# Performance work log

Measured on AMD Instinct MI355X. Metric: run time of the kernel, lower is better.

The kernel has to match this reference:

```python
import jax, jax.numpy as jnp
import numpy as np

D = 256            # number of graph nodes (example.size(3))
K1 = D // 2        # topkpool1 k
K2 = D // 4        # topkpool2 k
B = 8


def _lrelu(x):
    return jnp.where(x > 0, x, 0.33 * x)


def _e2e(h, wa, ba, wb, bb):
    # h: [B,C,d,d]; wa,wb: [P,C,d] (squeezed (1,d)/(d,1) conv kernels)
    # cnn1: contract over columns j -> [B,P,d]; cnn2: contract over rows i -> [B,P,d]
    a = jnp.einsum('bcij,pcj->bpi', h, wa) + ba[None, :, None]
    b = jnp.einsum('bcij,pci->bpj', h, wb) + bb[None, :, None]
    # cat([a]*d, 3) + cat([b]*d, 2)  ==  broadcast-add
    return a[:, :, :, None] + b[:, :, None, :]


def _gcn(h, g, W, b):
    # h: [B,N,F_in], g: [B,N,N]; faithful to norm_g: g[i,j] / deg[j] (column-normalized
    # because torch broadcasts the [N] degree vector over the LAST dim)
    gb = (g > 0).astype(h.dtype)
    deg = gb.sum(axis=2)                      # [B,N] row sums
    gn = gb / deg[:, None, :]                 # divide column j by deg[j]
    return jnp.einsum('bij,bjf->bif', gn, h) @ W.T + b


def _pool(h, g, s, k):
    # h: [B,N,F], g: [B,N,N], s: [B,N,1] -> top-k nodes by score (descending)
    vals, idx = jax.lax.top_k(s[:, :, 0], k)              # [B,k]
    hn = jnp.take_along_axis(h, idx[:, :, None], axis=1)  # [B,k,F]
    gn = jnp.take_along_axis(g, idx[:, :, None], axis=1)
    gn = jnp.take_along_axis(gn, idx[:, None, :], axis=2) # [B,k,k]
    return hn, gn, vals[:, :, None]


def _readout(h):
    # h: [B,N,F] (node axis = 1); torch ReadOut on [B,F,N,1] max/mean over dim=2
    return jnp.concatenate([h.max(axis=1), h.mean(axis=1)], axis=1)  # [B,2F]


def _forward(x, w1a, b1a, w1b, b1b, w2a, b2a, w2b, b2b, e2n_w, e2n_b,
             a11_w, a11_b, a12_w, a12_b, g1_w, g1_b,
             a21_w, a21_b, a22_w, a22_b,
             d1_w, d1_b, d2_w, d2_b, d3_w, d3_b):
    h = _lrelu(_e2e(x, w1a, b1a, w1b, b1b))         # [B,128,d,d]
    h = _lrelu(_e2e(h, w2a, b2a, w2b, b2b))         # [B,256,d,d]
    # E2N conv (1,d): [B,8,d,1] -> node features [B,d,8]
    nodes = _lrelu(jnp.einsum('bcij,pcj->bpi', h, e2n_w) + e2n_b[None, :, None])
    nodes = jnp.transpose(nodes, (0, 2, 1))          # [B,d,8]
    g0 = x[:, 0]                                     # [B,d,d]

    w = _lrelu(_gcn(nodes, g0, a11_w, a11_b))        # [B,d,1]
    w = jax.nn.sigmoid(_gcn(w, g0, a12_w, a12_b))
    h1, g1, s1 = _pool(nodes, g0, w, K1)             # [B,K1,8], [B,K1,K1], [B,K1,1]
    out = h1 * s1 + h1
    sum1 = _readout(out)                             # [B,16]

    h2 = _gcn(out, g1, g1_w, g1_b)                   # [B,K1,8] (no activation, as in torch)
    w = _lrelu(_gcn(h2, g1, a21_w, a21_b))
    w = jax.nn.sigmoid(_gcn(w, g1, a22_w, a22_b))
    h3, g2, s2 = _pool(h2, g1, w, K2)                # [B,K2,8]
    out2 = h3 * s2 + h3
    sum2 = _readout(out2)                            # [B,16]

    z = sum1 + sum2                                  # [B,16]
    z = _lrelu(z @ d1_w.T + d1_b)                    # dropout = identity (eval mode)
    z = _lrelu(z @ d2_w.T + d2_b)
    return z @ d3_w.T + d3_b                         # [B,1]


def setup_inputs() -> dict:
    key = jax.random.key(0)
    ks = jax.random.split(key, 16)
    f32 = jnp.float32

    def rn(k, shape, scale):
        return jax.random.normal(k, shape, dtype=f32) * scale

    return {
        'x': jax.random.normal(ks[0], (B, 1, D, D), dtype=f32),
        'w1a': rn(ks[1], (128, 1, D), 0.08),  'b1a': jnp.zeros((128,), f32),
        'w1b': rn(ks[2], (128, 1, D), 0.08),  'b1b': jnp.zeros((128,), f32),
        'w2a': rn(ks[3], (256, 128, D), 0.008), 'b2a': jnp.zeros((256,), f32),
        'w2b': rn(ks[4], (256, 128, D), 0.008), 'b2b': jnp.zeros((256,), f32),
        'e2n_w': rn(ks[5], (8, 256, D), 0.005), 'e2n_b': jnp.zeros((8,), f32),
        'a11_w': rn(ks[6], (1, 8), 0.3),  'a11_b': jnp.zeros((1,), f32),
        'a12_w': rn(ks[7], (1, 1), 0.3),  'a12_b': jnp.zeros((1,), f32),
        'g1_w': rn(ks[8], (8, 8), 0.3),   'g1_b': jnp.zeros((8,), f32),
        'a21_w': rn(ks[9], (1, 8), 0.3),  'a21_b': jnp.zeros((1,), f32),
        'a22_w': rn(ks[10], (1, 1), 0.3), 'a22_b': jnp.zeros((1,), f32),
        'd1_w': rn(ks[11], (128, 16), 0.2), 'd1_b': jnp.zeros((128,), f32),
        'd2_w': rn(ks[12], (64, 128), 0.08), 'd2_b': jnp.zeros((64,), f32),
        'd3_w': rn(ks[13], (1, 64), 0.1),  'd3_b': jnp.zeros((1,), f32),
    }


def reference(x, w1a, b1a, w1b, b1b, w2a, b2a, w2b, b2b, e2n_w, e2n_b,
              a11_w, a11_b, a12_w, a12_b, g1_w, g1_b,
              a21_w, a21_b, a22_w, a22_b,
              d1_w, d1_b, d2_w, d2_b, d3_w, d3_b):
    return _forward(x, w1a, b1a, w1b, b1b, w2a, b2a, w2b, b2b, e2n_w, e2n_b,
                    a11_w, a11_b, a12_w, a12_b, g1_w, g1_b,
                    a21_w, a21_b, a22_w, a22_b,
                    d1_w, d1_b, d2_w, d2_b, d3_w, d3_b)
```

## Files before the change

kernel.cpp:

```cpp
#include <hip/hip_runtime.h>

typedef short s16x8 __attribute__((ext_vector_type(8)));
typedef float f32x4 __attribute__((ext_vector_type(4)));
typedef float f32x2 __attribute__((ext_vector_type(2)));

#define TID threadIdx.x

__device__ __forceinline__ float lrelu_f(float x) { return fmaxf(x, 0.33f * x); }

__device__ __forceinline__ unsigned lrelu_pack(float pv, f32x2 q) {
    f32x2 s = q + pv;
    f32x2 m = s * 0.33f;
    f32x2 r = __builtin_elementwise_max(s, m);
    unsigned u;
    asm("v_cvt_pk_bf16_f32 %0, %1, %2" : "=v"(u) : "v"(r.x), "v"(r.y));
    return u;
}
__device__ __forceinline__ unsigned pk_bf16(float a, float b) {
    unsigned u;
    asm("v_cvt_pk_bf16_f32 %0, %1, %2" : "=v"(u) : "v"(a), "v"(b));
    return u;
}

union FragU { s16x8 v; uint4 q; unsigned w[4]; };

__global__ __launch_bounds__(256) void k_convert(
    const float* __restrict__ sa, unsigned short* __restrict__ da, int na4,
    const float* __restrict__ sb, unsigned short* __restrict__ db, int nb4,
    const float* __restrict__ sc, unsigned short* __restrict__ dc, int nc4)
{
    const float* s; unsigned short* d; int n4;
    if (blockIdx.y == 0)      { s = sa; d = da; n4 = na4; }
    else if (blockIdx.y == 1) { s = sb; d = db; n4 = nb4; }
    else                      { s = sc; d = dc; n4 = nc4; }
    const int stride = gridDim.x * 256;
    for (int i = blockIdx.x * 256 + TID; i < n4; i += stride) {
        float4 v = ((const float4*)s)[i];
        ((uint2*)d)[i] = make_uint2(pk_bf16(v.x, v.y), pk_bf16(v.z, v.w));
    }
}

__global__ __launch_bounds__(128) void k_l1(
    const float* __restrict__ x,
    const float* __restrict__ w1a, const float* __restrict__ b1a,
    const float* __restrict__ w1b, const float* __restrict__ b1b,
    float* __restrict__ A1, float* __restrict__ B1)
{
    const int r = blockIdx.x, b = blockIdx.y, v = blockIdx.z;
    const int tid = TID;
    __shared__ float xr[256];
    const float* xb = x + b * 65536;
    if (v == 0) {
        xr[tid]       = xb[r * 256 + tid];
        xr[tid + 128] = xb[r * 256 + tid + 128];
    } else {
        xr[tid]       = xb[tid * 256 + r];
        xr[tid + 128] = xb[(tid + 128) * 256 + r];
    }
    __syncthreads();
    const float* w    = v ? w1b : w1a;
    const float* bias = v ? b1b : b1a;
    float* OUT = v ? B1 : A1;
    float acc = bias[tid];
    const float* wr = w + tid * 256;
    #pragma unroll 4
    for (int q = 0; q < 256; q += 8) {
        float4 a = *(const float4*)(wr + q);
        float4 c = *(const float4*)(wr + q + 4);
        acc += xr[q + 0] * a.x + xr[q + 1] * a.y + xr[q + 2] * a.z + xr[q + 3] * a.w;
        acc += xr[q + 4] * c.x + xr[q + 5] * c.y + xr[q + 6] * c.z + xr[q + 7] * c.w;
    }
    OUT[b * 32768 + tid * 256 + r] = acc;
}

__global__ __launch_bounds__(512, 4) void k_e2e(
    const float* __restrict__ A1, const float* __restrict__ B1,
    const unsigned short* __restrict__ w2aM, const unsigned short* __restrict__ w2bM,
    float* __restrict__ part)
{
    const int bid = blockIdx.x;
    const int xcd = bid & 7, tt = bid >> 3;
    const int hi = tt >> 5, inner = tt & 31;
    const int slice = xcd + 8 * hi;
    const int s = slice >> 1, which = slice & 1;
    const int rt = inner >> 3, b = inner & 7;
    const int bw = b * 2 + which;

    const float* P = (which ? B1 : A1) + b * 32768;
    const float* Q = (which ? A1 : B1) + b * 32768;
    const unsigned short* W = which ? w2bM : w2aM;
    const int c0 = s * 16, r0 = rt * 64;

    __shared__ float Qs[16][256];
    __shared__ float Ps[16][64];
    __shared__ uint4 Hs[2048];

    const int tid = TID;
    const int wave = tid >> 6, lane = tid & 63, quad = lane >> 4, l16 = lane & 15;
    const int pbase = wave * 32;

    {
        const float4* Qg = (const float4*)(Q + c0 * 256);
        float4* Qd = (float4*)&Qs[0][0];
        Qd[tid]       = Qg[tid];
        Qd[tid + 512] = Qg[tid + 512];
        int row = tid >> 5, c2 = (tid & 31) * 2;
        *(float2*)&Ps[row][c2] = *(const float2*)&P[(c0 + row) * 256 + r0 + c2];
    }
    __syncthreads();

    {
        const int qb = wave * 32 + quad * 8;
        f32x2 qp0 = *(const f32x2*)&Qs[0][qb + 0];
        f32x2 qp1 = *(const f32x2*)&Qs[0][qb + 2];
        f32x2 qp2 = *(const f32x2*)&Qs[0][qb + 4];
        f32x2 qp3 = *(const f32x2*)&Qs[0][qb + 6];
        #pragma unroll
        for (int rf = 0; rf < 4; ++rf) {
            float pv = Ps[0][rf * 16 + l16];
            uint4 u;
            u.x = lrelu_pack(pv, qp0);
            u.y = lrelu_pack(pv, qp1);
            u.z = lrelu_pack(pv, qp2);
            u.w = lrelu_pack(pv, qp3);
            Hs[(wave * 4 + rf) * 64 + lane] = u;
        }
    }

    f32x4 acc[2][4] = {};
    const unsigned short* Wrow[2];
    #pragma unroll
    for (int pf = 0; pf < 2; ++pf)
        Wrow[pf] = W + (size_t)(pbase + pf * 16 + l16) * 32768 + c0 * 256 + quad * 8;

    FragU af[2][2];
    #pragma unroll
    for (int pf = 0; pf < 2; ++pf) af[0][pf].q = *(const uint4*)(Wrow[pf]);

    __syncthreads();

    for (int c = 0; c < 16; ++c) {
        FragU hbf[2][4];
        #pragma unroll
        for (int nf = 0; nf < 4; ++nf)
            hbf[0][nf].q = Hs[nf * 64 + lane];

        #pragma unroll
        for (int q0 = 0; q0 < 8; ++q0) {
            const int cur = q0 & 1, nxt = cur ^ 1;
            const int cn = c + ((q0 + 1) >> 3), qn = (q0 + 1) & 7;
            if (cn < 16) {
                #pragma unroll
                for (int pf = 0; pf < 2; ++pf)
                    af[nxt][pf].q = *(const uint4*)(Wrow[pf] + cn * 256 + qn * 32);
            }
            if (q0 < 7) {
                #pragma unroll
                for (int nf = 0; nf < 4; ++nf)
                    hbf[nxt][nf].q = Hs[((q0 + 1) * 4 + nf) * 64 + lane];
            }
            #pragma unroll
            for (int nf = 0; nf < 4; ++nf)
                #pragma unroll
                for (int pf = 0; pf < 2; ++pf)
                    acc[pf][nf] = __builtin_amdgcn_mfma_f32_16x16x32_bf16(af[cur][pf].v, hbf[cur][nf].v, acc[pf][nf], 0, 0, 0);
        }
        __syncthreads();
        if (c + 1 < 16) {
            const int qb = wave * 32 + quad * 8;
            f32x2 qp0 = *(const f32x2*)&Qs[c + 1][qb + 0];
            f32x2 qp1 = *(const f32x2*)&Qs[c + 1][qb + 2];
            f32x2 qp2 = *(const f32x2*)&Qs[c + 1][qb + 4];
            f32x2 qp3 = *(const f32x2*)&Qs[c + 1][qb + 6];
            #pragma unroll
            for (int rf = 0; rf < 4; ++rf) {
                float pv = Ps[c + 1][rf * 16 + l16];
                uint4 u;
                u.x = lrelu_pack(pv, qp0);
                u.y = lrelu_pack(pv, qp1);
                u.z = lrelu_pack(pv, qp2);
                u.w = lrelu_pack(pv, qp3);
                Hs[(wave * 4 + rf) * 64 + lane] = u;
            }
            __syncthreads();
        }
    }

    float* pb = part + (size_t)(s * 16 + bw) * 65536;
    #pragma unroll
    for (int pf = 0; pf < 2; ++pf)
        #pragma unroll
        for (int nf = 0; nf < 4; ++nf)
            #pragma unroll
            for (int t = 0; t < 4; ++t) {
                int p = pbase + pf * 16 + quad * 4 + t;
                int r = r0 + nf * 16 + l16;
                pb[p * 256 + r] = acc[pf][nf][t];
            }
}

__global__ __launch_bounds__(256) void k_red(
    const float* __restrict__ part,
    const float* __restrict__ b2a, const float* __restrict__ b2b,
    float* __restrict__ A2, float* __restrict__ B2)
{
    const int bw = blockIdx.y; const int b = bw >> 1, which = bw & 1;
    const int idx = blockIdx.x * 256 + TID;
    const float4* pp = (const float4*)part;
    float4 acc = make_float4(0.f, 0.f, 0.f, 0.f);
    #pragma unroll
    for (int s = 0; s < 8; ++s) {
        float4 v = pp[(size_t)(s * 16 + bw) * 16384 + idx];
        acc.x += v.x; acc.y += v.y; acc.z += v.z; acc.w += v.w;
    }
    const int p = idx >> 6;
    const float bias = (which ? b2b : b2a)[p];
    acc.x += bias; acc.y += bias; acc.z += bias; acc.w += bias;
    float* OUT = (which ? B2 : A2) + b * 65536;
    ((float4*)OUT)[idx] = acc;
}

__global__ __launch_bounds__(256) void k_e2n(
    const float* __restrict__ A2, const float* __restrict__ B2,
    const unsigned short* __restrict__ e2nw,
    float* __restrict__ nodes_raw)
{
    const int it = blockIdx.x, b = blockIdx.y, sn = blockIdx.z;
    const int tid = TID, wave = tid >> 6, lane = tid & 63, quad = lane >> 4, l16 = lane & 15;
    const int i0 = it * 16;
    const int c0 = sn * 32 + wave * 8;
    const float* Ab = A2 + b * 65536;
    const float* Bb = B2 + b * 65536;
    const float* Brow0 = Bb + c0 * 256 + quad * 8;
    const unsigned short* Wrow0 = e2nw + (size_t)l16 * 65536 + c0 * 256 + quad * 8;

    f32x4 acc = {};
    FragU af[2];
    f32x2 qp[2][4];
    float pv, pvn;

    if (l16 < 8) af[0].q = *(const uint4*)(Wrow0);
    else         af[0].q = make_uint4(0u, 0u, 0u, 0u);
    #pragma unroll
    for (int k = 0; k < 4; ++k) qp[0][k] = *(const f32x2*)(Brow0 + 2 * k);
    pv = Ab[c0 * 256 + i0 + l16];

    for (int cc = 0; cc < 8; ++cc) {
        #pragma unroll
        for (int q0 = 0; q0 < 8; ++q0) {
            const int cur = q0 & 1, nxt = cur ^ 1;
            const int cn = (q0 == 7) ? cc + 1 : cc;
            const int qn = (q0 + 1) & 7;
            if (cn < 8) {
                if (l16 < 8) af[nxt].q = *(const uint4*)(Wrow0 + cn * 256 + qn * 32);
                else         af[nxt].q = make_uint4(0u, 0u, 0u, 0u);
                #pragma unroll
                for (int k = 0; k < 4; ++k)
                    qp[nxt][k] = *(const f32x2*)(Brow0 + cn * 256 + qn * 32 + 2 * k);
            }
            if (q0 == 4 && cc + 1 < 8) pvn = Ab[(c0 + cc + 1) * 256 + i0 + l16];
            FragU hb;
            hb.w[0] = lrelu_pack(pv, qp[cur][0]);
            hb.w[1] = lrelu_pack(pv, qp[cur][1]);
            hb.w[2] = lrelu_pack(pv, qp[cur][2]);
            hb.w[3] = lrelu_pack(pv, qp[cur][3]);
            acc = __builtin_amdgcn_mfma_f32_16x16x32_bf16(af[cur].v, hb.v, acc, 0, 0, 0);
            if (q0 == 7) pv = pvn;
        }
    }
    __shared__ float red[4][16][16];
    #pragma unroll
    for (int t = 0; t < 4; ++t) red[wave][quad * 4 + t][l16] = acc[t];
    __syncthreads();
    const int row = tid >> 4, col = tid & 15;
    if (row < 8) {
        float ssum = red[0][row][col] + red[1][row][col] + red[2][row][col] + red[3][row][col];
        atomicAdd(&nodes_raw[b * 2048 + (i0 + col) * 8 + row], ssum);
    }
}

__global__ __launch_bounds__(256) void k_adj(
    const float* __restrict__ x,
    unsigned long long* __restrict__ adjw, float* __restrict__ rdegw)
{
    const int b = blockIdx.y;
    const int tid = TID, wave = tid >> 6, lane = tid & 63;
    const int rbase = blockIdx.x * 32 + wave * 8;
    for (int rr = 0; rr < 8; ++rr) {
        const int row = rbase + rr;
        int d = 0;
        unsigned long long w[4];
        #pragma unroll
        for (int k = 0; k < 4; ++k) {
            float v = x[b * 65536 + row * 256 + k * 64 + lane];
            w[k] = __ballot(v > 0.0f);
            d += __popcll(w[k]);
        }
        if (lane == 0) {
            #pragma unroll
            for (int k = 0; k < 4; ++k) adjw[(b * 256 + row) * 4 + k] = w[k];
            rdegw[b * 256 + row] = d ? 1.0f / (float)d : 0.0f;
        }
    }
}

__global__ __launch_bounds__(256) void k_tail(
    const unsigned long long* __restrict__ adjw, const float* __restrict__ rdegw,
    const float* __restrict__ nodes_raw, const float* __restrict__ e2n_b,
    const float* __restrict__ a11_w, const float* __restrict__ a11_b,
    const float* __restrict__ a12_w, const float* __restrict__ a12_b,
    const float* __restrict__ g1_w,  const float* __restrict__ g1_b,
    const float* __restrict__ a21_w, const float* __restrict__ a21_b,
    const float* __restrict__ a22_w, const float* __restrict__ a22_b,
    const float* __restrict__ d1_w,  const float* __restrict__ d1_b,
    const float* __restrict__ d2_w,  const float* __restrict__ d2_b,
    const float* __restrict__ d3_w,  const float* __restrict__ d3_b,
    float* __restrict__ out)
{
    const int b = blockIdx.x;
    const int tid = TID;

    __shared__ unsigned long long adj[256][4];
    __shared__ float nod[256][8];
    __shared__ float rdeg[256];
    __shared__ float md[256];
    __shared__ float w1s[256];
    __shared__ float w2s[256];
    __shared__ int   selflag[256];
    __shared__ int   selidx[128];
    __shared__ float s1v[128];
    __shared__ float out1[128][8];
    __shared__ float aggL[128][8];
    __shared__ float h2L[128][8];
    __shared__ unsigned long long adj1[128][2];
    __shared__ float rdeg1[128];
    __shared__ float tA[128];
    __shared__ float w1t[128];
    __shared__ float w2t[128];
    __shared__ int   sel2flag[128];
    __shared__ int   sel2idx[64];
    __shared__ float s2v[64];
    __shared__ float out2[64][8];
    __shared__ float r1[16], r2[16], zz[16];
    __shared__ float z1[128];
    __shared__ float z2[64];

    if (tid < 128) { selidx[tid] = 0; s1v[tid] = 0.0f; }
    if (tid < 64)  { sel2idx[tid] = 0; s2v[tid] = 0.0f; }

    {
        #pragma unroll
        for (int k = 0; k < 4; ++k) adj[tid][k] = adjw[(b * 256 + tid) * 4 + k];
        rdeg[tid] = rdegw[b * 256 + tid];
        for (int f = 0; f < 8; ++f)
            nod[tid][f] = lrelu_f(nodes_raw[b * 2048 + tid * 8 + f] + e2n_b[f]);
    }
    __syncthreads();
    {
        float s = 0.0f;
        for (int f = 0; f < 8; ++f) s += nod[tid][f] * a11_w[f];
        md[tid] = s * rdeg[tid];
    }
    __syncthreads();
    {
        float s = 0.0f;
        for (int k = 0; k < 4; ++k) {
            unsigned long long m = adj[tid][k];
            while (m) { int j = __builtin_ctzll(m); m &= m - 1; s += md[k * 64 + j]; }
        }
        w1s[tid] = lrelu_f(s + a11_b[0]);
    }
    __syncthreads();
    md[tid] = w1s[tid] * a12_w[0] * rdeg[tid];
    __syncthreads();
    {
        float s = 0.0f;
        for (int k = 0; k < 4; ++k) {
            unsigned long long m = adj[tid][k];
            while (m) { int j = __builtin_ctzll(m); m &= m - 1; s += md[k * 64 + j]; }
        }
        w2s[tid] = 1.0f / (1.0f + expf(-(s + a12_b[0])));
    }
    __syncthreads();
    {
        const float my = w2s[tid];
        int cnt = 0;
        for (int j = 0; j < 256; ++j) {
            float o = w2s[j];
            cnt += (o > my) || (o == my && j < tid);
        }
        selflag[tid] = (cnt < 128) ? 1 : 0;
    }
    __syncthreads();
    if (selflag[tid]) {
        int pos = 0;
        for (int j = 0; j < tid; ++j) pos += selflag[j];
        if (pos < 128) { selidx[pos] = tid; s1v[pos] = w2s[tid]; }
    }
    __syncthreads();
    for (int k = tid; k < 1024; k += 256) {
        int t = k >> 3, f = k & 7;
        out1[t][f] = nod[selidx[t]][f] * (1.0f + s1v[t]);
    }
    __syncthreads();
    if (tid < 16) {
        int f = tid & 7;
        if (tid < 8) {
            float mx = -INFINITY;
            for (int t = 0; t < 128; ++t) mx = fmaxf(mx, out1[t][f]);
            r1[tid] = mx;
        } else {
            float s = 0.0f;
            for (int t = 0; t < 128; ++t) s += out1[t][f];
            r1[tid] = s * (1.0f / 128.0f);
        }
    }
    if (tid < 128) {
        unsigned long long wds[2] = {0ull, 0ull};
        const int gi = selidx[tid];
        for (int u = 0; u < 128; ++u) {
            const int gj = selidx[u];
            unsigned long long bit = (adj[gi][gj >> 6] >> (gj & 63)) & 1ull;
            wds[u >> 6] |= bit << (u & 63);
        }
        adj1[tid][0] = wds[0]; adj1[tid][1] = wds[1];
        int d = __popcll(wds[0]) + __popcll(wds[1]);
        rdeg1[tid] = d ? 1.0f / (float)d : 0.0f;
    }
    __syncthreads();
    {
        const int t = tid >> 1, f0 = (tid & 1) * 4;
        float a0 = 0, a1 = 0, a2 = 0, a3 = 0;
        for (int k = 0; k < 2; ++k) {
            unsigned long long m = adj1[t][k];
            while (m) {
                int u = __builtin_ctzll(m); m &= m - 1;
                int uu = k * 64 + u;
                float rr = rdeg1[uu];
                a0 += out1[uu][f0 + 0] * rr;
                a1 += out1[uu][f0 + 1] * rr;
                a2 += out1[uu][f0 + 2] * rr;
                a3 += out1[uu][f0 + 3] * rr;
            }
        }
        aggL[t][f0 + 0] = a0; aggL[t][f0 + 1] = a1; aggL[t][f0 + 2] = a2; aggL[t][f0 + 3] = a3;
    }
    __syncthreads();
    for (int k = tid; k < 1024; k += 256) {
        int t = k >> 3, fo = k & 7;
        float s = g1_b[fo];
        for (int f = 0; f < 8; ++f) s += aggL[t][f] * g1_w[fo * 8 + f];
        h2L[t][fo] = s;
    }
    __syncthreads();
    if (tid < 128) {
        float s = 0.0f;
        for (int f = 0; f < 8; ++f) s += h2L[tid][f] * a21_w[f];
        tA[tid] = s * rdeg1[tid];
    }
    __syncthreads();
    if (tid < 128) {
        float s = 0.0f;
        for (int k = 0; k < 2; ++k) {
            unsigned long long m = adj1[tid][k];
            while (m) { int u = __builtin_ctzll(m); m &= m - 1; s += tA[k * 64 + u]; }
        }
        w1t[tid] = lrelu_f(s + a21_b[0]);
    }
    __syncthreads();
    if (tid < 128) tA[tid] = w1t[tid] * a22_w[0] * rdeg1[tid];
    __syncthreads();
    if (tid < 128) {
        float s = 0.0f;
        for (int k = 0; k < 2; ++k) {
            unsigned long long m = adj1[tid][k];
            while (m) { int u = __builtin_ctzll(m); m &= m - 1; s += tA[k * 64 + u]; }
        }
        w2t[tid] = 1.0f / (1.0f + expf(-(s + a22_b[0])));
    }
    __syncthreads();
    if (tid < 128) {
        const float my = w2t[tid];
        int cnt = 0;
        for (int u = 0; u < 128; ++u) {
            float o = w2t[u];
            cnt += (o > my) || (o == my && u < tid);
        }
        sel2flag[tid] = (cnt < 64) ? 1 : 0;
    }
    __syncthreads();
    if (tid < 128 && sel2flag[tid]) {
        int pos = 0;
        for (int u = 0; u < tid; ++u) pos += sel2flag[u];
        if (pos < 64) { sel2idx[pos] = tid; s2v[pos] = w2t[tid]; }
    }
    __syncthreads();
    for (int k = tid; k < 512; k += 256) {
        int u = k >> 3, f = k & 7;
        out2[u][f] = h2L[sel2idx[u]][f] * (1.0f + s2v[u]);
    }
    __syncthreads();
    if (tid < 16) {
        int f = tid & 7;
        if (tid < 8) {
            float mx = -INFINITY;
            for (int t = 0; t < 64; ++t) mx = fmaxf(mx, out2[t][f]);
            r2[tid] = mx;
        } else {
            float s = 0.0f;
            for (int t = 0; t < 64; ++t) s += out2[t][f];
            r2[tid] = s * (1.0f / 64.0f);
        }
    }
    __syncthreads();
    if (tid < 16) zz[tid] = r1[tid] + r2[tid];
    __syncthreads();
    if (tid < 128) {
        float s = d1_b[tid];
        for (int k = 0; k < 16; ++k) s += zz[k] * d1_w[tid * 16 + k];
        z1[tid] = lrelu_f(s);
    }
    __syncthreads();
    if (tid < 64) {
        float s = d2_b[tid];
        for (int k = 0; k < 128; ++k) s += z1[k] * d2_w[tid * 128 + k];
        z2[tid] = lrelu_f(s);
    }
    __syncthreads();
    if (tid == 0) {
        float s = d3_b[0];
        for (int k = 0; k < 64; ++k) s += z2[k] * d3_w[k];
        out[b] = s;
    }
}

extern "C" void kernel_launch(void* const* d_in, const int* in_sizes, int n_in,
                              void* d_out, int out_size, void* d_ws, size_t ws_size,
                              hipStream_t stream) {
    const float* x     = (const float*)d_in[0];
    const float* w1a   = (const float*)d_in[1];
    const float* b1a   = (const float*)d_in[2];
    const float* w1b   = (const float*)d_in[3];
    const float* b1b   = (const float*)d_in[4];
    const float* w2a   = (const float*)d_in[5];
    const float* b2a   = (const float*)d_in[6];
    const float* w2b   = (const float*)d_in[7];
    const float* b2b   = (const float*)d_in[8];
    const float* e2nw  = (const float*)d_in[9];

    float* ws        = (float*)d_ws;
    float* A1        = ws;
    float* B1        = ws + 262144;
    float* A2        = ws + 524288;
    float* B2        = ws + 1048576;
    float* nodes_raw = ws + 1572864;
    float* rdegw     = ws + 1589248;
    unsigned long long* adjw = (unsigned long long*)(ws + 1597440);
    float* part      = ws + 1613824;
    unsigned short* w2aM  = (unsigned short*)(ws + 10002432);
    unsigned short* w2bM  = w2aM + 8388608;
    unsigned short* e2nwM = w2bM + 8388608;

    k_convert<<<dim3(512, 3), 256, 0, stream>>>(
        w2a, w2aM, 8388608 / 4,
        w2b, w2bM, 8388608 / 4,
        e2nw, e2nwM, 524288 / 4);
    hipMemsetAsync(nodes_raw, 0, 16384 * sizeof(float), stream);
    k_l1<<<dim3(256, 8, 2), 128, 0, stream>>>(x, w1a, b1a, w1b, b1b, A1, B1);
    k_adj<<<dim3(8, 8), 256, 0, stream>>>(x, adjw, rdegw);
    k_e2e<<<dim3(512), 512, 0, stream>>>(A1, B1, w2aM, w2bM, part);
    k_red<<<dim3(64, 16), 256, 0, stream>>>(part, b2a, b2b, A2, B2);
    k_e2n<<<dim3(16, 8, 8), 256, 0, stream>>>(A2, B2, e2nwM, nodes_raw);
    k_tail<<<dim3(8), 256, 0, stream>>>(adjw, rdegw, nodes_raw, (const float*)d_in[10],
        (const float*)d_in[11], (const float*)d_in[12], (const float*)d_in[13], (const float*)d_in[14],
        (const float*)d_in[15], (const float*)d_in[16], (const float*)d_in[17], (const float*)d_in[18],
        (const float*)d_in[19], (const float*)d_in[20], (const float*)d_in[21], (const float*)d_in[22],
        (const float*)d_in[23], (const float*)d_in[24], (const float*)d_in[25], (const float*)d_in[26],
        (float*)d_out);
}
```

Measured before the change: 441.2 us.

## Merge weight conversion, layer-1, adjacency and memset into one front kernel

Replaces the separate convert, memset, layer-1 and adjacency launches with a single block-partitioned front kernel, cutting launch overhead and letting these independent jobs run concurrently. The B1 path of layer 1 is rewritten as a tiled GEMM that loads x tiles coalesced into shared memory, replacing the strided column gather used before. The A1 path now packs two rows per 256-thread block. The cost is a larger kernel with mixed block roles and possible load imbalance between them.

```diff
diff --git a/kernel.cpp b/kernel.cpp
--- a/kernel.cpp
+++ b/kernel.cpp
@@ -24,53 +24,114 @@
 
 union FragU { s16x8 v; uint4 q; unsigned w[4]; };
 
-__global__ __launch_bounds__(256) void k_convert(
-    const float* __restrict__ sa, unsigned short* __restrict__ da, int na4,
-    const float* __restrict__ sb, unsigned short* __restrict__ db, int nb4,
-    const float* __restrict__ sc, unsigned short* __restrict__ dc, int nc4)
-{
-    const float* s; unsigned short* d; int n4;
-    if (blockIdx.y == 0)      { s = sa; d = da; n4 = na4; }
-    else if (blockIdx.y == 1) { s = sb; d = db; n4 = nb4; }
-    else                      { s = sc; d = dc; n4 = nc4; }
-    const int stride = gridDim.x * 256;
-    for (int i = blockIdx.x * 256 + TID; i < n4; i += stride) {
-        float4 v = ((const float4*)s)[i];
-        ((uint2*)d)[i] = make_uint2(pk_bf16(v.x, v.y), pk_bf16(v.z, v.w));
-    }
-}
-
-__global__ __launch_bounds__(128) void k_l1(
+__global__ __launch_bounds__(256) void k_front(
     const float* __restrict__ x,
+    const float* __restrict__ w2a, unsigned short* __restrict__ w2aM,
+    const float* __restrict__ w2b, unsigned short* __restrict__ w2bM,
+    const float* __restrict__ e2nw, unsigned short* __restrict__ e2nwM,
     const float* __restrict__ w1a, const float* __restrict__ b1a,
     const float* __restrict__ w1b, const float* __restrict__ b1b,
-    float* __restrict__ A1, float* __restrict__ B1)
+    float* __restrict__ A1, float* __restrict__ B1,
+    unsigned long long* __restrict__ adjw, float* __restrict__ rdegw,
+    float* __restrict__ nodes_raw)
 {
-    const int r = blockIdx.x, b = blockIdx.y, v = blockIdx.z;
+    const int bid = blockIdx.x;
     const int tid = TID;
-    __shared__ float xr[256];
-    const float* xb = x + b * 65536;
-    if (v == 0) {
-        xr[tid]       = xb[r * 256 + tid];
-        xr[tid + 128] = xb[r * 256 + tid + 128];
+
+    __shared__ float xr[2][256];
+    __shared__ float xs[64][36];
+
+    if (bid < 1536) {
+        const int which = bid >> 9;
+        const int inner = bid & 511;
+        const float* s; unsigned short* d; int n4;
+        if (which == 0)      { s = w2a;  d = w2aM;  n4 = 2097152; }
+        else if (which == 1) { s = w2b;  d = w2bM;  n4 = 2097152; }
+        else                 { s = e2nw; d = e2nwM; n4 = 131072; }
+        for (int i = inner * 256 + tid; i < n4; i += 131072) {
+            float4 v = ((const float4*)s)[i];
+            ((uint2*)d)[i] = make_uint2(pk_bf16(v.x, v.y), pk_bf16(v.z, v.w));
+        }
+    } else if (bid < 2560) {
+        const int idx = bid - 1536;
+        const int rp = idx & 127, b = idx >> 7;
+        const int h = tid >> 7, ctid = tid & 127;
+        const int r = rp * 2 + h;
+        const float* xb = x + b * 65536;
+        xr[h][ctid]       = xb[r * 256 + ctid];
+        xr[h][ctid + 128] = xb[r * 256 + ctid + 128];
+        __syncthreads();
+        float acc = b1a[ctid];
+        const float* wr = w1a + ctid * 256;
+        #pragma unroll 4
+        for (int q = 0; q < 256; q += 8) {
+            float4 a = *(const float4*)(wr + q);
+            float4 c = *(const float4*)(wr + q + 4);
+            acc += xr[h][q + 0] * a.x + xr[h][q + 1] * a.y + xr[h][q + 2] * a.z + xr[h][q + 3] * a.w;
+            acc += xr[h][q + 4] * c.x + xr[h][q + 5] * c.y + xr[h][q + 6] * c.z + xr[h][q + 7] * c.w;
+        }
+        A1[b * 32768 + ctid * 256 + r] = acc;
+    } else if (bid < 2624) {
+        const int idx = bid - 2560;
+        const int jt = idx & 7, b = idx >> 3;
+        const int c = tid & 127, jh = tid >> 7;
+        const float* xb = x + b * 65536;
+        float acc[16];
+        #pragma unroll
+        for (int jj = 0; jj < 16; ++jj) acc[jj] = 0.0f;
+        for (int ch = 0; ch < 4; ++ch) {
+            const int i0 = ch * 64;
+            {
+                const int row = tid >> 2, seg = tid & 3;
+                const float* src = xb + (i0 + row) * 256 + jt * 32 + seg * 8;
+                float4 a0 = *(const float4*)src;
+                float4 a1 = *(const float4*)(src + 4);
+                *(float4*)&xs[row][seg * 8]     = a0;
+                *(float4*)&xs[row][seg * 8 + 4] = a1;
+            }
+            __syncthreads();
+            const float* wrow = w1b + c * 256 + i0;
+            #pragma unroll
+            for (int i4 = 0; i4 < 64; i4 += 4) {
+                float4 wv = *(const float4*)(wrow + i4);
+                #pragma unroll
+                for (int u = 0; u < 4; ++u) {
+                    const float wsc = (u == 0) ? wv.x : (u == 1) ? wv.y : (u == 2) ? wv.z : wv.w;
+                    const float* xrow = &xs[i4 + u][jh * 16];
+                    #pragma unroll
+                    for (int jj = 0; jj < 16; ++jj)
+                        acc[jj] += wsc * xrow[jj];
+                }
+            }
+            __syncthreads();
+        }
+        const float bias = b1b[c];
+        float* outp = B1 + b * 32768 + c * 256 + jt * 32 + jh * 16;
+        #pragma unroll
+        for (int jj = 0; jj < 16; ++jj) outp[jj] = acc[jj] + bias;
     } else {
-        xr[tid]       = xb[tid * 256 + r];
-        xr[tid + 128] = xb[(tid + 128) * 256 + r];
-    }
-    __syncthreads();
-    const float* w    = v ? w1b : w1a;
-    const float* bias = v ? b1b : b1a;
-    float* OUT = v ? B1 : A1;
-    float acc = bias[tid];
-    const float* wr = w + tid * 256;
-    #pragma unroll 4
-    for (int q = 0; q < 256; q += 8) {
-        float4 a = *(const float4*)(wr + q);
-        float4 c = *(const float4*)(wr + q + 4);
-        acc += xr[q + 0] * a.x + xr[q + 1] * a.y + xr[q + 2] * a.z + xr[q + 3] * a.w;
-        acc += xr[q + 4] * c.x + xr[q + 5] * c.y + xr[q + 6] * c.z + xr[q + 7] * c.w;
-    }
-    OUT[b * 32768 + tid * 256 + r] = acc;
+        const int idx = bid - 2624;
+        nodes_raw[idx * 256 + tid] = 0.0f;
+        const int gx = idx & 7, b = idx >> 3;
+        const int wv = tid >> 6, lane = tid & 63;
+        const int rbase = gx * 32 + wv * 8;
+        for (int rr = 0; rr < 8; ++rr) {
+            const int row = rbase + rr;
+            int d = 0;
+            unsigned long long w[4];
+            #pragma unroll
+            for (int k = 0; k < 4; ++k) {
+                float v = x[b * 65536 + row * 256 + k * 64 + lane];
+                w[k] = __ballot(v > 0.0f);
+                d += __popcll(w[k]);
+            }
+            if (lane == 0) {
+                #pragma unroll
+                for (int k = 0; k < 4; ++k) adjw[(b * 256 + row) * 4 + k] = w[k];
+                rdegw[b * 256 + row] = d ? 1.0f / (float)d : 0.0f;
+            }
+        }
+    }
 }
 
 __global__ __launch_bounds__(512, 4) void k_e2e(
@@ -276,31 +337,6 @@
     if (row < 8) {
         float ssum = red[0][row][col] + red[1][row][col] + red[2][row][col] + red[3][row][col];
         atomicAdd(&nodes_raw[b * 2048 + (i0 + col) * 8 + row], ssum);
-    }
-}
-
-__global__ __launch_bounds__(256) void k_adj(
-    const float* __restrict__ x,
-    unsigned long long* __restrict__ adjw, float* __restrict__ rdegw)
-{
-    const int b = blockIdx.y;
-    const int tid = TID, wave = tid >> 6, lane = tid & 63;
-    const int rbase = blockIdx.x * 32 + wave * 8;
-    for (int rr = 0; rr < 8; ++rr) {
-        const int row = rbase + rr;
-        int d = 0;
-        unsigned long long w[4];
-        #pragma unroll
-        for (int k = 0; k < 4; ++k) {
-            float v = x[b * 65536 + row * 256 + k * 64 + lane];
-            w[k] = __ballot(v > 0.0f);
-            d += __popcll(w[k]);
-        }
-        if (lane == 0) {
-            #pragma unroll
-            for (int k = 0; k < 4; ++k) adjw[(b * 256 + row) * 4 + k] = w[k];
-            rdegw[b * 256 + row] = d ? 1.0f / (float)d : 0.0f;
-        }
     }
 }
 
@@ -561,13 +597,9 @@
     unsigned short* w2bM  = w2aM + 8388608;
     unsigned short* e2nwM = w2bM + 8388608;
 
-    k_convert<<<dim3(512, 3), 256, 0, stream>>>(
-        w2a, w2aM, 8388608 / 4,
-        w2b, w2bM, 8388608 / 4,
-        e2nw, e2nwM, 524288 / 4);
-    hipMemsetAsync(nodes_raw, 0, 16384 * sizeof(float), stream);
-    k_l1<<<dim3(256, 8, 2), 128, 0, stream>>>(x, w1a, b1a, w1b, b1b, A1, B1);
-    k_adj<<<dim3(8, 8), 256, 0, stream>>>(x, adjw, rdegw);
+    k_front<<<dim3(2688), 256, 0, stream>>>(
+        x, w2a, w2aM, w2b, w2bM, e2nw, e2nwM,
+        w1a, b1a, w1b, b1b, A1, B1, adjw, rdegw, nodes_raw);
     k_e2e<<<dim3(512), 512, 0, stream>>>(A1, B1, w2aM, w2bM, part);
     k_red<<<dim3(64, 16), 256, 0, stream>>>(part, b2a, b2b, A2, B2);
     k_e2n<<<dim3(16, 8, 8), 256, 0, stream>>>(A2, B2, e2nwM, nodes_raw);
```

Measured after the change: 428.1 us. 1.03x faster.
